# Performance work log

Measured on AMD Instinct MI355X. Metric: run time of the kernel, lower is better.

Reference implementation:

```python
import jax, jax.numpy as jnp
import numpy as np

B, T, E, H, M2 = 8, 2048, 256, 2, 134
HD = E // H


def setup_inputs() -> dict:
    key = jax.random.key(0)
    ks = jax.random.split(key, 10)
    s = 0.02
    return {
        "X": jax.random.normal(ks[0], (B, T, E), dtype=jnp.float32),
        "Y": jax.random.uniform(ks[1], (B, M2), dtype=jnp.float32),
        "wpe": s * jax.random.normal(ks[2], (T, E), dtype=jnp.float32),
        "ln1_g": jnp.ones((E,), jnp.float32), "ln1_b": jnp.zeros((E,), jnp.float32),
        "attn_w": s * jax.random.normal(ks[3], (3 * E, E), dtype=jnp.float32),
        "attn_b": jnp.zeros((3 * E,), jnp.float32),
        "attnproj_w": s * jax.random.normal(ks[4], (E, E), dtype=jnp.float32),
        "attnproj_b": jnp.zeros((E,), jnp.float32),
        "ln2_g": jnp.ones((E,), jnp.float32), "ln2_b": jnp.zeros((E,), jnp.float32),
        "fc_w": s * jax.random.normal(ks[5], (2 * E, E), dtype=jnp.float32),
        "fc_b": jnp.zeros((2 * E,), jnp.float32),
        "mlpproj_w": s * jax.random.normal(ks[6], (E, 2 * E), dtype=jnp.float32),
        "mlpproj_b": jnp.zeros((E,), jnp.float32),
        "lnf_g": jnp.ones((E,), jnp.float32), "lnf_b": jnp.zeros((E,), jnp.float32),
        "head_w": s * jax.random.normal(ks[7], (M2, E), dtype=jnp.float32),
        "head_b": jnp.zeros((M2,), jnp.float32),
    }


def _ln(x, g, b, eps=1e-5):
    mu = x.mean(-1, keepdims=True)
    var = ((x - mu) ** 2).mean(-1, keepdims=True)
    return (x - mu) * jax.lax.rsqrt(var + eps) * g + b


def reference(X, Y, wpe, ln1_g, ln1_b, attn_w, attn_b, attnproj_w, attnproj_b,
              ln2_g, ln2_b, fc_w, fc_b, mlpproj_w, mlpproj_b, lnf_g, lnf_b,
              head_w, head_b):
    # positional ids = arange(T) -> wpe itself; cls ids = [0]*T/2 + [1]*T/2
    cls_ids = np.concatenate([np.zeros(T // 2, np.int32), np.ones(T // 2, np.int32)])
    x = X + wpe + wpe[cls_ids]                      # [B,T,E] (dropout = identity, eval)

    # single Block (n_layer=1), preceded by ReLU as in cross_mod loop
    x = jax.nn.relu(x)
    h = _ln(x, ln1_g, ln1_b)
    qkv = h @ attn_w.T + attn_b                     # [B,T,3E]
    q, k, v = jnp.split(qkv, 3, axis=-1)
    q, k, v = jax.nn.relu(q), jax.nn.relu(k), jax.nn.relu(v)
    split_heads = lambda t: t.reshape(B, T, H, HD).transpose(0, 2, 1, 3)
    q, k, v = split_heads(q), split_heads(k), split_heads(v)
    att = jnp.einsum('bhqd,bhkd->bhqk', q, k) * (1.0 / np.sqrt(HD))
    tril = jnp.tril(jnp.ones((T, T), dtype=bool))
    # masked_fill(-inf) then ReLU  ==  zero outside causal mask, ReLU inside
    att = jnp.where(tril, jax.nn.relu(att), 0.0)    # [B,H,T,T]
    y = jnp.einsum('bhqk,bhkd->bhqd', att, v)
    y = y.transpose(0, 2, 1, 3).reshape(B, T, E)
    x = x + (y @ attnproj_w.T + attnproj_b)

    h = _ln(x, ln2_g, ln2_b)
    x = x + (jax.nn.relu(h @ fc_w.T + fc_b) @ mlpproj_w.T + mlpproj_b)

    x = jax.nn.relu(x)
    x = _ln(x, lnf_g, lnf_b)
    x = jax.nn.relu(x)
    emb = x.mean(axis=1)                            # [B,E]
    logits = jax.nn.relu(emb @ head_w.T + head_b)   # [B,M2]

    loss1 = jnp.sqrt(jnp.mean((logits - Y) ** 2))
    e1, e2 = emb[:, : E // 2], emb[:, E // 2:]
    loss3 = jnp.sqrt(jnp.mean((e1 - e2) ** 2))
    loss = 50.0 * loss1 + loss3
    return (e1, e2, loss, loss1, loss3, logits)
```

## Files before the change

### kernel.cpp

```cpp
#include <hip/hip_runtime.h>
#include <hip/hip_bf16.h>

#define Bc 8
#define Tc 2048
#define Ec 256
#define Hc 2
#define HDc 128
#define Mrows (Bc*Tc)
#define M2c 134

using bfx8  = __attribute__((ext_vector_type(8))) __bf16;
using f32x4 = __attribute__((ext_vector_type(4))) float;

__device__ __forceinline__ void gll16(const __bf16* g, __bf16* lds) {
    __builtin_amdgcn_global_load_lds(
        (const __attribute__((address_space(1))) unsigned int*)g,
        (__attribute__((address_space(3))) unsigned int*)lds, 16, 0, 0);
}

__global__ __launch_bounds__(256) void prep_k(const float* attn_w, const float* apw,
                                              const float* fcw, const float* mpw,
                                              __bf16* wb, float* embsum) {
    int i = blockIdx.x * 256 + threadIdx.x;
    if (i < 2048) embsum[i] = 0.f;
    if (i < 196608)       wb[i] = (__bf16)attn_w[i];
    else if (i < 262144)  wb[i] = (__bf16)apw[i - 196608];
    else if (i < 393216)  wb[i] = (__bf16)fcw[i - 262144];
    else if (i < 524288)  wb[i] = (__bf16)mpw[i - 393216];
}

__global__ __launch_bounds__(256) void embed_ln_k(const float* X, const float* wpe,
                                                  const float* g, const float* bb,
                                                  __bf16* xres, __bf16* hb) {
    int m = blockIdx.x;
    int t = m & (Tc - 1);
    int e = threadIdx.x;
    float v = X[(size_t)m * Ec + e] + wpe[(size_t)t * Ec + e] + wpe[(size_t)(t >= 1024) * Ec + e];
    v = fmaxf(v, 0.f);
    xres[(size_t)m * Ec + e] = (__bf16)v;
    float s1 = v, s2 = v * v;
    #pragma unroll
    for (int o = 32; o; o >>= 1) { s1 += __shfl_xor(s1, o, 64); s2 += __shfl_xor(s2, o, 64); }
    __shared__ float a1[4], a2[4];
    int w = threadIdx.x >> 6;
    if ((threadIdx.x & 63) == 0) { a1[w] = s1; a2[w] = s2; }
    __syncthreads();
    float m1 = (a1[0] + a1[1] + a1[2] + a1[3]) * (1.f / 256.f);
    float m2 = (a2[0] + a2[1] + a2[2] + a2[3]) * (1.f / 256.f);
    float r = rsqrtf(m2 - m1 * m1 + 1e-5f);
    hb[(size_t)m * Ec + e] = (__bf16)((v - m1) * r * g[e] + bb[e]);
}

template <int EPI>
__global__ __launch_bounds__(256) void gemm_bt(const __bf16* __restrict__ A,
                                               const __bf16* __restrict__ Bw,
                                               const float* __restrict__ bias,
                                               int N, int K,
                                               __bf16* __restrict__ outb,
                                               __bf16* __restrict__ Qb,
                                               __bf16* __restrict__ Kb,
                                               __bf16* __restrict__ Vb) {
    __shared__ __bf16 As[128 * 64];
    __shared__ __bf16 Bs[128 * 64];
    const int tid = threadIdx.x, w = tid >> 6, l = tid & 63;
    const int m0 = blockIdx.y * 128, n0 = blockIdx.x * 128;
    const int wr = w >> 1, wc = w & 1;
    const int quad = l >> 4, col15 = l & 15;

    f32x4 acc[4][4];
    f32x4 zz = {0.f, 0.f, 0.f, 0.f};
    #pragma unroll
    for (int i = 0; i < 4; i++)
        #pragma unroll
        for (int j = 0; j < 4; j++) acc[i][j] = zz;

    const int lrow = l >> 3;
    const int pbs  = l & 7;

    for (int kb = 0; kb < K; kb += 64) {
        #pragma unroll
        for (int it = 0; it < 4; it++) {
            int chunk = w * 4 + it;
            int row = chunk * 8 + lrow;
            int lb = pbs ^ (row & 7);
            gll16(A  + (size_t)(m0 + row) * K + kb + lb * 8, As + chunk * 512);
            gll16(Bw + (size_t)(n0 + row) * K + kb + lb * 8, Bs + chunk * 512);
        }
        __syncthreads();
        #pragma unroll
        for (int ks = 0; ks < 2; ks++) {
            bfx8 af[4], bfr[4];
            #pragma unroll
            for (int rt = 0; rt < 4; rt++) {
                int row = wr * 64 + rt * 16 + col15;
                int pb = (ks * 4 + quad) ^ (row & 7);
                af[rt] = *(const bfx8*)(As + row * 64 + pb * 8);
            }
            #pragma unroll
            for (int ct = 0; ct < 4; ct++) {
                int row = wc * 64 + ct * 16 + col15;
                int pb = (ks * 4 + quad) ^ (row & 7);
                bfr[ct] = *(const bfx8*)(Bs + row * 64 + pb * 8);
            }
            #pragma unroll
            for (int rt = 0; rt < 4; rt++)
                #pragma unroll
                for (int ct = 0; ct < 4; ct++)
                    acc[rt][ct] = __builtin_amdgcn_mfma_f32_16x16x32_bf16(af[rt], bfr[ct], acc[rt][ct], 0, 0, 0);
        }
        __syncthreads();
    }

    #pragma unroll
    for (int rt = 0; rt < 4; rt++)
        #pragma unroll
        for (int ct = 0; ct < 4; ct++) {
            int mgb = m0 + wr * 64 + rt * 16 + quad * 4;
            int ng  = n0 + wc * 64 + ct * 16 + col15;
            float bsv = bias[ng];
            #pragma unroll
            for (int r = 0; r < 4; r++) {
                float val = acc[rt][ct][r] + bsv;
                int mg = mgb + r;
                if constexpr (EPI == 0) {
                    val = fmaxf(val, 0.f);
                    int sel = ng >> 8;
                    int hh = (ng >> 7) & 1;
                    int d = ng & 127;
                    int bb = mg >> 11, tt = mg & (Tc - 1);
                    size_t idx = ((size_t)((bb * 2 + hh) * Tc + tt)) * HDc + d;
                    __bf16 bv = (__bf16)val;
                    if (sel == 0) Qb[idx] = bv;
                    else if (sel == 1) Kb[idx] = bv;
                    else Vb[idx] = bv;
                } else {
                    outb[(size_t)mg * 512 + ng] = (__bf16)fmaxf(val, 0.f);
                }
            }
        }
}

__global__ __launch_bounds__(256) void transpose_v(const unsigned short* Vb, unsigned short* Vt) {
    __shared__ unsigned short tile[64][66];
    int kt = blockIdx.x, dt = blockIdx.y, bh = blockIdx.z;
    int tid = threadIdx.x;
    int k0 = kt * 64, d0 = dt * 64;
    int rr = tid >> 4, cc = (tid & 15) * 4;
    #pragma unroll
    for (int p = 0; p < 4; p++) {
        int k = p * 16 + rr;
        const unsigned short* src = Vb + ((size_t)(bh * Tc + k0 + k)) * HDc + d0 + cc;
        ushort4 vv = *(const ushort4*)src;
        tile[k][cc] = vv.x; tile[k][cc + 1] = vv.y; tile[k][cc + 2] = vv.z; tile[k][cc + 3] = vv.w;
    }
    __syncthreads();
    #pragma unroll
    for (int p = 0; p < 4; p++) {
        int d = p * 16 + rr;
        unsigned short* dst = Vt + ((size_t)(bh * HDc + d0 + d)) * Tc + k0 + cc;
        ushort4 ov;
        ov.x = tile[cc][d]; ov.y = tile[cc + 1][d]; ov.z = tile[cc + 2][d]; ov.w = tile[cc + 3][d];
        *(ushort4*)dst = ov;
    }
}

__global__ __launch_bounds__(256, 4) void attn6_k(const __bf16* __restrict__ Qb,
                                                  const __bf16* __restrict__ Kb,
                                                  const __bf16* __restrict__ Vt,
                                                  __bf16* __restrict__ Y1,
                                                  __bf16* __restrict__ Y2,
                                                  __bf16* __restrict__ Y3,
                                                  __bf16* __restrict__ Y4) {
    __shared__ __bf16 Ks[64 * 128];
    __shared__ __bf16 Vs[128 * 64];
    __shared__ __bf16 Ss[64 * 64];
    int bid = blockIdx.x;
    int lane8 = bid & 7;
    int s = bid >> 3;
    int bh = ((s & 1) << 3) | lane8;
    int f = s >> 1;
    int qt, ch;
    if (f < 8)       { qt = f;                    ch = 0; }
    else if (f < 24) { qt = 8 + ((f - 8) >> 1);   ch = (f - 8) & 1; }
    else if (f < 48) { int r = f - 24; int d3 = r / 3; qt = 16 + d3; ch = r - 3 * d3; }
    else             { int r = f - 48; qt = 24 + (r >> 2); ch = r & 3; }
    int Q0 = qt * 64;
    int kts = ch * 8;
    int kte = min(kts + 8, qt + 1);

    int tid = threadIdx.x, w = tid >> 6, l = tid & 63;
    int quad = l >> 4, col15 = l & 15;
    const int lrowK = l >> 4, pbsK = l & 15;
    const int lrowV = l >> 3, pbsV = l & 7;

    #pragma unroll
    for (int it = 0; it < 4; it++) {
        int chunk = w * 4 + it;
        int row = chunk * 4 + lrowK;
        int lb = pbsK ^ (row & 7);
        gll16(Qb + ((size_t)(bh * Tc + Q0 + row)) * HDc + lb * 8, Ks + chunk * 512);
    }
    __syncthreads();
    bfx8 qf[4];
    #pragma unroll
    for (int ks = 0; ks < 4; ks++) {
        int row = w * 16 + col15;
        int pb = (ks * 4 + quad) ^ (row & 7);
        qf[ks] = *(const bfx8*)(Ks + row * 128 + pb * 8);
    }

    f32x4 zz = {0.f, 0.f, 0.f, 0.f};
    f32x4 yacc[8];
    #pragma unroll
    for (int i = 0; i < 8; i++) yacc[i] = zz;

    for (int kt = kts; kt < kte; kt++) {
        __syncthreads();
        #pragma unroll
        for (int it = 0; it < 4; it++) {
            int chunk = w * 4 + it;
            int rowK = chunk * 4 + lrowK;
            int lbK = pbsK ^ (rowK & 7);
            gll16(Kb + ((size_t)(bh * Tc + kt * 64 + rowK)) * HDc + lbK * 8, Ks + chunk * 512);
            int rowV = chunk * 8 + lrowV;
            int lbV = pbsV ^ (rowV & 7);
            gll16(Vt + ((size_t)(bh * HDc + rowV)) * Tc + kt * 64 + lbV * 8, Vs + chunk * 512);
        }
        __syncthreads();

        f32x4 sacc[4];
        #pragma unroll
        for (int i = 0; i < 4; i++) sacc[i] = zz;
        #pragma unroll
        for (int ks = 0; ks < 4; ks++) {
            #pragma unroll
            for (int ct = 0; ct < 4; ct++) {
                int row = ct * 16 + col15;
                int pb = (ks * 4 + quad) ^ (row & 7);
                bfx8 kf = *(const bfx8*)(Ks + row * 128 + pb * 8);
                sacc[ct] = __builtin_amdgcn_mfma_f32_16x16x32_bf16(qf[ks], kf, sacc[ct], 0, 0, 0);
            }
        }

        #pragma unroll
        for (int ct = 0; ct < 4; ct++) {
            int kl = ct * 16 + col15;
            int kg = kt * 64 + kl;
            int blk = kl >> 3, off = kl & 7;
            #pragma unroll
            for (int r = 0; r < 4; r++) {
                int qlw = w * 16 + quad * 4 + r;
                float val = (kg <= Q0 + qlw) ? fmaxf(sacc[ct][r], 0.f) : 0.f;
                int pb = blk ^ (qlw & 7);
                Ss[qlw * 64 + pb * 8 + off] = (__bf16)val;
            }
        }

        #pragma unroll
        for (int ks = 0; ks < 2; ks++) {
            int rowS = w * 16 + col15;
            int pbS = (ks * 4 + quad) ^ (rowS & 7);
            bfx8 sf = *(const bfx8*)(Ss + rowS * 64 + pbS * 8);
            #pragma unroll
            for (int dt = 0; dt < 8; dt++) {
                int row = dt * 16 + col15;
                int pb = (ks * 4 + quad) ^ (row & 7);
                bfx8 vf = *(const bfx8*)(Vs + row * 64 + pb * 8);
                yacc[dt] = __builtin_amdgcn_mfma_f32_16x16x32_bf16(sf, vf, yacc[dt], 0, 0, 0);
            }
        }
    }

    __bf16* Yp = (ch == 0) ? Y1 : (ch == 1) ? Y2 : (ch == 2) ? Y3 : Y4;
    int b = bh >> 1, h = bh & 1;
    const float sc = 0.08838834764831845f;
    #pragma unroll
    for (int dt = 0; dt < 8; dt++) {
        int d = dt * 16 + col15;
        #pragma unroll
        for (int r = 0; r < 4; r++) {
            int q = Q0 + w * 16 + quad * 4 + r;
            Yp[((size_t)(b * Tc + q)) * Ec + h * HDc + d] = (__bf16)(yacc[dt][r] * sc);
        }
    }
}

template <int MODE>
__global__ __launch_bounds__(256) void gemm_ln(const __bf16* __restrict__ A,
                                               const __bf16* __restrict__ A2,
                                               const __bf16* __restrict__ A3,
                                               const __bf16* __restrict__ A4,
                                               const __bf16* __restrict__ W,
                                               const float* __restrict__ bias, int K,
                                               const __bf16* __restrict__ resid,
                                               const float* __restrict__ g,
                                               const float* __restrict__ bb,
                                               __bf16* __restrict__ out1,
                                               __bf16* __restrict__ out2,
                                               float* __restrict__ embsum) {
    __shared__ __bf16 As[64 * 64];
    __shared__ __bf16 Bs[256 * 64];
    __shared__ float cs[256];
    const int tid = threadIdx.x, w = tid >> 6, l = tid & 63;
    const int m0 = blockIdx.x * 64;
    const int quad = l >> 4, col15 = l & 15;
    const int lrow = l >> 3, pbs = l & 7;

    f32x4 acc[16];
    f32x4 zz = {0.f, 0.f, 0.f, 0.f};
    #pragma unroll
    for (int i = 0; i < 16; i++) acc[i] = zz;
    if (MODE == 1) { cs[tid] = 0.f; }

    int nsum = 1;
    if (MODE == 0) nsum = (((m0 & (Tc - 1)) >> 6) + 8) >> 3;
    const __bf16* Ys[4] = {A, A2, A3, A4};

    for (int kb = 0; kb < K; kb += 64) {
        if (MODE == 0) {
            bfx8 av[2];
            int rows[2], blks[2];
            #pragma unroll
            for (int it = 0; it < 2; it++) {
                int idx = it * 256 + tid;
                int row = idx >> 3, blk = idx & 7;
                rows[it] = row; blks[it] = blk;
                size_t off = (size_t)(m0 + row) * K + kb + blk * 8;
                bfx8 a1 = *(const bfx8*)(A + off);
                float tmp[8];
                #pragma unroll
                for (int jj = 0; jj < 8; jj++) tmp[jj] = (float)a1[jj];
                for (int j = 1; j < nsum; j++) {
                    bfx8 aj = *(const bfx8*)(Ys[j] + off);
                    #pragma unroll
                    for (int jj = 0; jj < 8; jj++) tmp[jj] += (float)aj[jj];
                }
                #pragma unroll
                for (int jj = 0; jj < 8; jj++) a1[jj] = (__bf16)tmp[jj];
                av[it] = a1;
            }
            __syncthreads();
            #pragma unroll
            for (int it = 0; it < 2; it++) {
                int row = rows[it];
                int pb = blks[it] ^ (row & 7);
                *(bfx8*)(As + row * 64 + pb * 8) = av[it];
            }
        } else {
            __syncthreads();
            #pragma unroll
            for (int it = 0; it < 2; it++) {
                int chunk = w * 2 + it;
                int row = chunk * 8 + lrow;
                int lb = pbs ^ (row & 7);
                gll16(A + (size_t)(m0 + row) * K + kb + lb * 8, As + chunk * 512);
            }
        }
        #pragma unroll
        for (int it = 0; it < 8; it++) {
            int chunk = w * 8 + it;
            int row = chunk * 8 + lrow;
            int lb = pbs ^ (row & 7);
            gll16(W + (size_t)row * K + kb + lb * 8, Bs + chunk * 512);
        }
        __syncthreads();
        #pragma unroll
        for (int ks = 0; ks < 2; ks++) {
            int arow = w * 16 + col15;
            int apb = (ks * 4 + quad) ^ (arow & 7);
            bfx8 af = *(const bfx8*)(As + arow * 64 + apb * 8);
            #pragma unroll
            for (int ct = 0; ct < 16; ct++) {
                int brow = ct * 16 + col15;
                int bpb = (ks * 4 + quad) ^ (brow & 7);
                bfx8 bf = *(const bfx8*)(Bs + brow * 64 + bpb * 8);
                acc[ct] = __builtin_amdgcn_mfma_f32_16x16x32_bf16(af, bf, acc[ct], 0, 0, 0);
            }
        }
    }
    __syncthreads();

    float xv[16][4];
    #pragma unroll
    for (int ct = 0; ct < 16; ct++) {
        int ng = ct * 16 + col15;
        float bsv = bias[ng];
        #pragma unroll
        for (int r = 0; r < 4; r++) {
            int mg = m0 + w * 16 + quad * 4 + r;
            float v = acc[ct][r] + bsv + (float)resid[(size_t)mg * 256 + ng];
            if (MODE == 1) v = fmaxf(v, 0.f);
            xv[ct][r] = v;
        }
    }
    if (MODE == 0) {
        #pragma unroll
        for (int ct = 0; ct < 16; ct++) {
            int ng = ct * 16 + col15;
            #pragma unroll
            for (int r = 0; r < 4; r++) {
                int mg = m0 + w * 16 + quad * 4 + r;
                out1[(size_t)mg * 256 + ng] = (__bf16)xv[ct][r];
            }
        }
    }
    float s1[4], s2[4];
    #pragma unroll
    for (int r = 0; r < 4; r++) {
        float a = 0.f, b2 = 0.f;
        #pragma unroll
        for (int ct = 0; ct < 16; ct++) { a += xv[ct][r]; b2 += xv[ct][r] * xv[ct][r]; }
        #pragma unroll
        for (int o = 1; o < 16; o <<= 1) { a += __shfl_xor(a, o, 64); b2 += __shfl_xor(b2, o, 64); }
        s1[r] = a; s2[r] = b2;
    }
    float colsum[16];
    #pragma unroll
    for (int ct = 0; ct < 16; ct++) colsum[ct] = 0.f;
    #pragma unroll
    for (int r = 0; r < 4; r++) {
        float mu = s1[r] * (1.f / 256.f);
        float var = s2[r] * (1.f / 256.f) - mu * mu;
        float rs = rsqrtf(var + 1e-5f);
        #pragma unroll
        for (int ct = 0; ct < 16; ct++) {
            int ng = ct * 16 + col15;
            float h = (xv[ct][r] - mu) * rs * g[ng] + bb[ng];
            if (MODE == 1) {
                colsum[ct] += fmaxf(h, 0.f);
            } else {
                int mg = m0 + w * 16 + quad * 4 + r;
                out2[(size_t)mg * 256 + ng] = (__bf16)h;
            }
        }
    }
    if (MODE == 1) {
        #pragma unroll
        for (int ct = 0; ct < 16; ct++) {
            colsum[ct] += __shfl_xor(colsum[ct], 16, 64);
            colsum[ct] += __shfl_xor(colsum[ct], 32, 64);
        }
        if (quad == 0) {
            #pragma unroll
            for (int ct = 0; ct < 16; ct++)
                atomicAdd(&cs[ct * 16 + col15], colsum[ct]);
        }
        __syncthreads();
        atomicAdd(&embsum[(m0 >> 11) * 256 + tid], cs[tid]);
    }
}

__global__ __launch_bounds__(256) void final_k(const float* embsum, const float* Yt,
                                               const float* head_w, const float* head_b,
                                               float* out) {
    __shared__ float semb[2048];
    __shared__ float slog[1072];
    int tid = threadIdx.x;
    for (int i = tid; i < 2048; i += 256) semb[i] = embsum[i] * (1.f / 2048.f);
    __syncthreads();
    float part1 = 0.f;
    for (int idx = tid; idx < 1072; idx += 256) {
        int b = idx / M2c, n = idx - b * M2c;
        float acc = head_b[n];
        const float* wn = head_w + (size_t)n * Ec;
        const float* e = semb + b * Ec;
        #pragma unroll 8
        for (int k = 0; k < Ec; k++) acc += e[k] * wn[k];
        acc = fmaxf(acc, 0.f);
        slog[idx] = acc;
        float d = acc - Yt[idx];
        part1 += d * d;
    }
    float part3 = 0.f;
    for (int idx = tid; idx < 1024; idx += 256) {
        int b = idx >> 7, i = idx & 127;
        float d = semb[b * Ec + i] - semb[b * Ec + 128 + i];
        part3 += d * d;
    }
    #pragma unroll
    for (int o = 32; o; o >>= 1) { part1 += __shfl_xor(part1, o, 64); part3 += __shfl_xor(part3, o, 64); }
    __shared__ float r1[4], r3[4];
    int w = tid >> 6;
    if ((tid & 63) == 0) { r1[w] = part1; r3[w] = part3; }
    __syncthreads();
    float l1 = sqrtf((r1[0] + r1[1] + r1[2] + r1[3]) / 1072.f);
    float l3 = sqrtf((r3[0] + r3[1] + r3[2] + r3[3]) / 1024.f);
    for (int idx = tid; idx < 1024; idx += 256) {
        int b = idx >> 7, i = idx & 127;
        out[idx]        = semb[b * Ec + i];
        out[1024 + idx] = semb[b * Ec + 128 + i];
    }
    if (tid == 0) {
        out[2048] = 50.f * l1 + l3;
        out[2049] = l1;
        out[2050] = l3;
    }
    for (int idx = tid; idx < 1072; idx += 256) out[2051 + idx] = slog[idx];
}

extern "C" void kernel_launch(void* const* d_in, const int* in_sizes, int n_in,
                              void* d_out, int out_size, void* d_ws, size_t ws_size,
                              hipStream_t stream) {
    const float* X        = (const float*)d_in[0];
    const float* Yt       = (const float*)d_in[1];
    const float* wpe      = (const float*)d_in[2];
    const float* ln1_g    = (const float*)d_in[3];
    const float* ln1_b    = (const float*)d_in[4];
    const float* attn_w   = (const float*)d_in[5];
    const float* attn_b   = (const float*)d_in[6];
    const float* apw      = (const float*)d_in[7];
    const float* apb      = (const float*)d_in[8];
    const float* ln2_g    = (const float*)d_in[9];
    const float* ln2_b    = (const float*)d_in[10];
    const float* fcw      = (const float*)d_in[11];
    const float* fcb      = (const float*)d_in[12];
    const float* mpw      = (const float*)d_in[13];
    const float* mpb      = (const float*)d_in[14];
    const float* lnf_g    = (const float*)d_in[15];
    const float* lnf_b    = (const float*)d_in[16];
    const float* head_w   = (const float*)d_in[17];
    const float* head_b   = (const float*)d_in[18];

    char* ws = (char*)d_ws;
    const size_t MB = 1048576;
    __bf16* xres   = (__bf16*)(ws + 0 * MB);
    __bf16* hb     = (__bf16*)(ws + 8 * MB);
    __bf16* Qb     = (__bf16*)(ws + 16 * MB);
    __bf16* Kb     = (__bf16*)(ws + 24 * MB);
    __bf16* Vb     = (__bf16*)(ws + 32 * MB);
    __bf16* Vt     = (__bf16*)(ws + 40 * MB);
    __bf16* Y1     = (__bf16*)(ws + 48 * MB);
    __bf16* Y2     = (__bf16*)(ws + 56 * MB);
    __bf16* fcout  = (__bf16*)(ws + 64 * MB);
    __bf16* wb     = (__bf16*)(ws + 80 * MB);
    float*  embsum = (float*)(ws + 81 * MB);

    __bf16* x2   = Qb;
    __bf16* h2   = Kb;
    __bf16* Y3   = hb;
    __bf16* Y4   = Vb;

    __bf16* wqkv = wb;
    __bf16* wap  = wb + 196608;
    __bf16* wfc  = wb + 262144;
    __bf16* wmp  = wb + 393216;

    prep_k<<<2048, 256, 0, stream>>>(attn_w, apw, fcw, mpw, wb, embsum);
    embed_ln_k<<<Mrows, 256, 0, stream>>>(X, wpe, ln1_g, ln1_b, xres, hb);
    gemm_bt<0><<<dim3(6, 128), 256, 0, stream>>>(hb, wqkv, attn_b, 768, 256,
                                                 nullptr, Qb, Kb, Vb);
    transpose_v<<<dim3(32, 2, 16), 256, 0, stream>>>((const unsigned short*)Vb, (unsigned short*)Vt);
    attn6_k<<<1280, 256, 0, stream>>>(Qb, Kb, Vt, Y1, Y2, Y3, Y4);
    gemm_ln<0><<<256, 256, 0, stream>>>(Y1, Y2, Y3, Y4, wap, apb, 256, xres, ln2_g, ln2_b,
                                        x2, h2, nullptr);
    gemm_bt<2><<<dim3(4, 128), 256, 0, stream>>>(h2, wfc, fcb, 512, 256,
                                                 fcout, nullptr, nullptr, nullptr);
    gemm_ln<1><<<256, 256, 0, stream>>>(fcout, nullptr, nullptr, nullptr, wmp, mpb, 512,
                                        x2, lnf_g, lnf_b, nullptr, nullptr, embsum);
    final_k<<<1, 256, 0, stream>>>(embsum, Yt, head_w, head_b, (float*)d_out);
}
```

Baseline: 256.6 us.

## Fuse attention-proj, LN2, MLP and final LN into one kernel; merge prep into embed

Replaces the three post-attention kernels (proj+LN2, fc GEMM, mlp-proj+LNf) with one kernel per 64-row tile. The LN2 output and the fc activations stay in LDS instead of going through global memory. The weight-conversion prep kernel is folded into the embedding/LN kernel to drop one launch. This removes intermediate HBM traffic and launches, but uses only 256 blocks at one block per CU with large LDS (~120KB), and each block re-streams all MLP weights through LDS.

```diff
diff --git a/kernel.cpp b/kernel.cpp
--- a/kernel.cpp
+++ b/kernel.cpp
@@ -18,23 +18,23 @@
         (__attribute__((address_space(3))) unsigned int*)lds, 16, 0, 0);
 }
 
-__global__ __launch_bounds__(256) void prep_k(const float* attn_w, const float* apw,
-                                              const float* fcw, const float* mpw,
-                                              __bf16* wb, float* embsum) {
-    int i = blockIdx.x * 256 + threadIdx.x;
-    if (i < 2048) embsum[i] = 0.f;
-    if (i < 196608)       wb[i] = (__bf16)attn_w[i];
-    else if (i < 262144)  wb[i] = (__bf16)apw[i - 196608];
-    else if (i < 393216)  wb[i] = (__bf16)fcw[i - 262144];
-    else if (i < 524288)  wb[i] = (__bf16)mpw[i - 393216];
-}
-
-__global__ __launch_bounds__(256) void embed_ln_k(const float* X, const float* wpe,
-                                                  const float* g, const float* bb,
-                                                  __bf16* xres, __bf16* hb) {
+__global__ __launch_bounds__(256) void embed_prep_k(const float* X, const float* wpe,
+                                                    const float* g, const float* bb,
+                                                    const float* attn_w, const float* apw,
+                                                    const float* fcw, const float* mpw,
+                                                    __bf16* wb, float* embsum,
+                                                    __bf16* xres, __bf16* hb) {
     int m = blockIdx.x;
+    int e = threadIdx.x;
+    if (m < 2048) {
+        int i = m * 256 + e;
+        if (i < 196608)       wb[i] = (__bf16)attn_w[i];
+        else if (i < 262144)  wb[i] = (__bf16)apw[i - 196608];
+        else if (i < 393216)  wb[i] = (__bf16)fcw[i - 262144];
+        else                  wb[i] = (__bf16)mpw[i - 393216];
+        if (m < 8) embsum[m * 256 + e] = 0.f;
+    }
     int t = m & (Tc - 1);
-    int e = threadIdx.x;
     float v = X[(size_t)m * Ec + e] + wpe[(size_t)t * Ec + e] + wpe[(size_t)(t >= 1024) * Ec + e];
     v = fmaxf(v, 0.f);
     xres[(size_t)m * Ec + e] = (__bf16)v;
@@ -51,15 +51,13 @@
     hb[(size_t)m * Ec + e] = (__bf16)((v - m1) * r * g[e] + bb[e]);
 }
 
-template <int EPI>
-__global__ __launch_bounds__(256) void gemm_bt(const __bf16* __restrict__ A,
-                                               const __bf16* __restrict__ Bw,
-                                               const float* __restrict__ bias,
-                                               int N, int K,
-                                               __bf16* __restrict__ outb,
-                                               __bf16* __restrict__ Qb,
-                                               __bf16* __restrict__ Kb,
-                                               __bf16* __restrict__ Vb) {
+__global__ __launch_bounds__(256) void gemm_qkv(const __bf16* __restrict__ A,
+                                                const __bf16* __restrict__ Bw,
+                                                const float* __restrict__ bias,
+                                                __bf16* __restrict__ Qb,
+                                                __bf16* __restrict__ Kb,
+                                                __bf16* __restrict__ Vb) {
+    const int K = 256;
     __shared__ __bf16 As[128 * 64];
     __shared__ __bf16 Bs[128 * 64];
     const int tid = threadIdx.x, w = tid >> 6, l = tid & 63;
@@ -120,22 +118,17 @@
             float bsv = bias[ng];
             #pragma unroll
             for (int r = 0; r < 4; r++) {
-                float val = acc[rt][ct][r] + bsv;
+                float val = fmaxf(acc[rt][ct][r] + bsv, 0.f);
                 int mg = mgb + r;
-                if constexpr (EPI == 0) {
-                    val = fmaxf(val, 0.f);
-                    int sel = ng >> 8;
-                    int hh = (ng >> 7) & 1;
-                    int d = ng & 127;
-                    int bb = mg >> 11, tt = mg & (Tc - 1);
-                    size_t idx = ((size_t)((bb * 2 + hh) * Tc + tt)) * HDc + d;
-                    __bf16 bv = (__bf16)val;
-                    if (sel == 0) Qb[idx] = bv;
-                    else if (sel == 1) Kb[idx] = bv;
-                    else Vb[idx] = bv;
-                } else {
-                    outb[(size_t)mg * 512 + ng] = (__bf16)fmaxf(val, 0.f);
-                }
+                int sel = ng >> 8;
+                int hh = (ng >> 7) & 1;
+                int d = ng & 127;
+                int bb = mg >> 11, tt = mg & (Tc - 1);
+                size_t idx = ((size_t)((bb * 2 + hh) * Tc + tt)) * HDc + d;
+                __bf16 bv = (__bf16)val;
+                if (sel == 0) Qb[idx] = bv;
+                else if (sel == 1) Kb[idx] = bv;
+                else Vb[idx] = bv;
             }
         }
 }
@@ -285,90 +278,82 @@
     }
 }
 
-template <int MODE>
-__global__ __launch_bounds__(256) void gemm_ln(const __bf16* __restrict__ A,
-                                               const __bf16* __restrict__ A2,
-                                               const __bf16* __restrict__ A3,
-                                               const __bf16* __restrict__ A4,
-                                               const __bf16* __restrict__ W,
-                                               const float* __restrict__ bias, int K,
-                                               const __bf16* __restrict__ resid,
-                                               const float* __restrict__ g,
-                                               const float* __restrict__ bb,
-                                               __bf16* __restrict__ out1,
-                                               __bf16* __restrict__ out2,
-                                               float* __restrict__ embsum) {
-    __shared__ __bf16 As[64 * 64];
+__global__ __launch_bounds__(256, 1) void mega_k(const __bf16* __restrict__ Y1,
+                                                 const __bf16* __restrict__ Y2,
+                                                 const __bf16* __restrict__ Y3,
+                                                 const __bf16* __restrict__ Y4,
+                                                 const __bf16* __restrict__ wap,
+                                                 const float* __restrict__ apb,
+                                                 const __bf16* __restrict__ xres,
+                                                 const float* __restrict__ ln2_g,
+                                                 const float* __restrict__ ln2_b,
+                                                 const __bf16* __restrict__ wfc,
+                                                 const float* __restrict__ fcb,
+                                                 const __bf16* __restrict__ wmp,
+                                                 const float* __restrict__ mpb,
+                                                 const float* __restrict__ lnf_g,
+                                                 const float* __restrict__ lnf_b,
+                                                 float* __restrict__ embsum) {
+    __shared__ __bf16 h2s[4 * 4096];
+    __shared__ __bf16 fc64[8 * 4096];
     __shared__ __bf16 Bs[256 * 64];
     __shared__ float cs[256];
     const int tid = threadIdx.x, w = tid >> 6, l = tid & 63;
     const int m0 = blockIdx.x * 64;
     const int quad = l >> 4, col15 = l & 15;
     const int lrow = l >> 3, pbs = l & 7;
+    f32x4 zz = {0.f, 0.f, 0.f, 0.f};
+    cs[tid] = 0.f;
+
+    int nsum = (((m0 & (Tc - 1)) >> 6) + 8) >> 3;
+    const __bf16* Ys[4] = {Y1, Y2, Y3, Y4};
+    __bf16* As = fc64;
 
     f32x4 acc[16];
-    f32x4 zz = {0.f, 0.f, 0.f, 0.f};
     #pragma unroll
     for (int i = 0; i < 16; i++) acc[i] = zz;
-    if (MODE == 1) { cs[tid] = 0.f; }
-
-    int nsum = 1;
-    if (MODE == 0) nsum = (((m0 & (Tc - 1)) >> 6) + 8) >> 3;
-    const __bf16* Ys[4] = {A, A2, A3, A4};
-
-    for (int kb = 0; kb < K; kb += 64) {
-        if (MODE == 0) {
-            bfx8 av[2];
-            int rows[2], blks[2];
-            #pragma unroll
-            for (int it = 0; it < 2; it++) {
-                int idx = it * 256 + tid;
-                int row = idx >> 3, blk = idx & 7;
-                rows[it] = row; blks[it] = blk;
-                size_t off = (size_t)(m0 + row) * K + kb + blk * 8;
-                bfx8 a1 = *(const bfx8*)(A + off);
-                float tmp[8];
+
+    for (int kb = 0; kb < 256; kb += 64) {
+        bfx8 av[2]; int rows[2], blks[2];
+        #pragma unroll
+        for (int it = 0; it < 2; it++) {
+            int idx = it * 256 + tid;
+            int row = idx >> 3, blk = idx & 7;
+            rows[it] = row; blks[it] = blk;
+            size_t off = (size_t)(m0 + row) * 256 + kb + blk * 8;
+            bfx8 a1 = *(const bfx8*)(Y1 + off);
+            float tmp[8];
+            #pragma unroll
+            for (int jj = 0; jj < 8; jj++) tmp[jj] = (float)a1[jj];
+            for (int j = 1; j < nsum; j++) {
+                bfx8 aj = *(const bfx8*)(Ys[j] + off);
                 #pragma unroll
-                for (int jj = 0; jj < 8; jj++) tmp[jj] = (float)a1[jj];
-                for (int j = 1; j < nsum; j++) {
-                    bfx8 aj = *(const bfx8*)(Ys[j] + off);
-                    #pragma unroll
-                    for (int jj = 0; jj < 8; jj++) tmp[jj] += (float)aj[jj];
-                }
-                #pragma unroll
-                for (int jj = 0; jj < 8; jj++) a1[jj] = (__bf16)tmp[jj];
-                av[it] = a1;
-            }
-            __syncthreads();
-            #pragma unroll
-            for (int it = 0; it < 2; it++) {
-                int row = rows[it];
-                int pb = blks[it] ^ (row & 7);
-                *(bfx8*)(As + row * 64 + pb * 8) = av[it];
-            }
-        } else {
-            __syncthreads();
-            #pragma unroll
-            for (int it = 0; it < 2; it++) {
-                int chunk = w * 2 + it;
-                int row = chunk * 8 + lrow;
-                int lb = pbs ^ (row & 7);
-                gll16(A + (size_t)(m0 + row) * K + kb + lb * 8, As + chunk * 512);
-            }
+                for (int jj = 0; jj < 8; jj++) tmp[jj] += (float)aj[jj];
+            }
+            #pragma unroll
+            for (int jj = 0; jj < 8; jj++) a1[jj] = (__bf16)tmp[jj];
+            av[it] = a1;
+        }
+        __syncthreads();
+        #pragma unroll
+        for (int it = 0; it < 2; it++) {
+            int row = rows[it];
+            int pb = blks[it] ^ (row & 7);
+            *(bfx8*)(As + row * 64 + pb * 8) = av[it];
         }
         #pragma unroll
         for (int it = 0; it < 8; it++) {
             int chunk = w * 8 + it;
             int row = chunk * 8 + lrow;
             int lb = pbs ^ (row & 7);
-            gll16(W + (size_t)row * K + kb + lb * 8, Bs + chunk * 512);
+            gll16(wap + (size_t)row * 256 + kb + lb * 8, Bs + chunk * 512);
         }
         __syncthreads();
         #pragma unroll
         for (int ks = 0; ks < 2; ks++) {
             int arow = w * 16 + col15;
-            int apb = (ks * 4 + quad) ^ (arow & 7);
-            bfx8 af = *(const bfx8*)(As + arow * 64 + apb * 8);
+            int apbk = (ks * 4 + quad) ^ (arow & 7);
+            bfx8 af = *(const bfx8*)(As + arow * 64 + apbk * 8);
             #pragma unroll
             for (int ct = 0; ct < 16; ct++) {
                 int brow = ct * 16 + col15;
@@ -378,31 +363,123 @@
             }
         }
     }
-    __syncthreads();
 
     float xv[16][4];
     #pragma unroll
     for (int ct = 0; ct < 16; ct++) {
         int ng = ct * 16 + col15;
-        float bsv = bias[ng];
+        float bsv = apb[ng];
         #pragma unroll
         for (int r = 0; r < 4; r++) {
             int mg = m0 + w * 16 + quad * 4 + r;
-            float v = acc[ct][r] + bsv + (float)resid[(size_t)mg * 256 + ng];
-            if (MODE == 1) v = fmaxf(v, 0.f);
-            xv[ct][r] = v;
-        }
-    }
-    if (MODE == 0) {
+            xv[ct][r] = acc[ct][r] + bsv + (float)xres[(size_t)mg * 256 + ng];
+        }
+    }
+    {
+        float s1[4], s2[4];
+        #pragma unroll
+        for (int r = 0; r < 4; r++) {
+            float a = 0.f, b2 = 0.f;
+            #pragma unroll
+            for (int ct = 0; ct < 16; ct++) { a += xv[ct][r]; b2 += xv[ct][r] * xv[ct][r]; }
+            #pragma unroll
+            for (int o = 1; o < 16; o <<= 1) { a += __shfl_xor(a, o, 64); b2 += __shfl_xor(b2, o, 64); }
+            s1[r] = a; s2[r] = b2;
+        }
+        #pragma unroll
+        for (int r = 0; r < 4; r++) {
+            float mu = s1[r] * (1.f / 256.f);
+            float var = s2[r] * (1.f / 256.f) - mu * mu;
+            float rs = rsqrtf(var + 1e-5f);
+            int row = w * 16 + quad * 4 + r;
+            #pragma unroll
+            for (int ct = 0; ct < 16; ct++) {
+                int ng = ct * 16 + col15;
+                float h = (xv[ct][r] - mu) * rs * ln2_g[ng] + ln2_b[ng];
+                int panel = ng >> 6, c = ng & 63;
+                h2s[panel * 4096 + row * 64 + ((c >> 3) ^ (row & 7)) * 8 + (c & 7)] = (__bf16)h;
+            }
+        }
+    }
+
+    for (int half = 0; half < 2; half++) {
+        f32x4 acc2[16];
+        #pragma unroll
+        for (int i = 0; i < 16; i++) acc2[i] = zz;
+        for (int kb = 0; kb < 256; kb += 64) {
+            __syncthreads();
+            #pragma unroll
+            for (int it = 0; it < 8; it++) {
+                int chunk = w * 8 + it;
+                int row = chunk * 8 + lrow;
+                int lb = pbs ^ (row & 7);
+                gll16(wfc + (size_t)(half * 256 + row) * 256 + kb + lb * 8, Bs + chunk * 512);
+            }
+            __syncthreads();
+            int panel = kb >> 6;
+            #pragma unroll
+            for (int ks = 0; ks < 2; ks++) {
+                int arow = w * 16 + col15;
+                int apbk = (ks * 4 + quad) ^ (arow & 7);
+                bfx8 af = *(const bfx8*)(h2s + panel * 4096 + arow * 64 + apbk * 8);
+                #pragma unroll
+                for (int ct = 0; ct < 16; ct++) {
+                    int brow = ct * 16 + col15;
+                    int bpb = (ks * 4 + quad) ^ (brow & 7);
+                    bfx8 bf = *(const bfx8*)(Bs + brow * 64 + bpb * 8);
+                    acc2[ct] = __builtin_amdgcn_mfma_f32_16x16x32_bf16(af, bf, acc2[ct], 0, 0, 0);
+                }
+            }
+        }
         #pragma unroll
         for (int ct = 0; ct < 16; ct++) {
-            int ng = ct * 16 + col15;
+            int col = half * 256 + ct * 16 + col15;
+            float bsv = fcb[col];
+            int panel = col >> 6, c = col & 63;
             #pragma unroll
             for (int r = 0; r < 4; r++) {
-                int mg = m0 + w * 16 + quad * 4 + r;
-                out1[(size_t)mg * 256 + ng] = (__bf16)xv[ct][r];
-            }
-        }
+                int row = w * 16 + quad * 4 + r;
+                float val = fmaxf(acc2[ct][r] + bsv, 0.f);
+                fc64[panel * 4096 + row * 64 + ((c >> 3) ^ (row & 7)) * 8 + (c & 7)] = (__bf16)val;
+            }
+        }
+    }
+
+    #pragma unroll
+    for (int i = 0; i < 16; i++) acc[i] = zz;
+    for (int kb = 0; kb < 512; kb += 64) {
+        __syncthreads();
+        #pragma unroll
+        for (int it = 0; it < 8; it++) {
+            int chunk = w * 8 + it;
+            int row = chunk * 8 + lrow;
+            int lb = pbs ^ (row & 7);
+            gll16(wmp + (size_t)row * 512 + kb + lb * 8, Bs + chunk * 512);
+        }
+        __syncthreads();
+        int panel = kb >> 6;
+        #pragma unroll
+        for (int ks = 0; ks < 2; ks++) {
+            int arow = w * 16 + col15;
+            int apbk = (ks * 4 + quad) ^ (arow & 7);
+            bfx8 af = *(const bfx8*)(fc64 + panel * 4096 + arow * 64 + apbk * 8);
+            #pragma unroll
+            for (int ct = 0; ct < 16; ct++) {
+                int brow = ct * 16 + col15;
+                int bpb = (ks * 4 + quad) ^ (brow & 7);
+                bfx8 bf = *(const bfx8*)(Bs + brow * 64 + bpb * 8);
+                acc[ct] = __builtin_amdgcn_mfma_f32_16x16x32_bf16(af, bf, acc[ct], 0, 0, 0);
+            }
+        }
+    }
+
+    #pragma unroll
+    for (int ct = 0; ct < 16; ct++) {
+        int ng = ct * 16 + col15;
+        float bsv = mpb[ng];
+        #pragma unroll
+        for (int r = 0; r < 4; r++)
+            xv[ct][r] = fmaxf(acc[ct][r] + bsv + xv[ct][r], 0.f);
     }
     float s1[4], s2[4];
     #pragma unroll
@@ -425,29 +502,22 @@
         #pragma unroll
         for (int ct = 0; ct < 16; ct++) {
             int ng = ct * 16 + col15;
-            float h = (xv[ct][r] - mu) * rs * g[ng] + bb[ng];
-            if (MODE == 1) {
-                colsum[ct] += fmaxf(h, 0.f);
-            } else {
-                int mg = m0 + w * 16 + quad * 4 + r;
-                out2[(size_t)mg * 256 + ng] = (__bf16)h;
-            }
-        }
-    }
-    if (MODE == 1) {
-        #pragma unroll
-        for (int ct = 0; ct < 16; ct++) {
-            colsum[ct] += __shfl_xor(colsum[ct], 16, 64);
-            colsum[ct] += __shfl_xor(colsum[ct], 32, 64);
-        }
-        if (quad == 0) {
-            #pragma unroll
-            for (int ct = 0; ct < 16; ct++)
-                atomicAdd(&cs[ct * 16 + col15], colsum[ct]);
-        }
-        __syncthreads();
-        atomicAdd(&embsum[(m0 >> 11) * 256 + tid], cs[tid]);
-    }
+            float h = (xv[ct][r] - mu) * rs * lnf_g[ng] + lnf_b[ng];
+            colsum[ct] += fmaxf(h, 0.f);
+        }
+    }
+    #pragma unroll
+    for (int ct = 0; ct < 16; ct++) {
+        colsum[ct] += __shfl_xor(colsum[ct], 16, 64);
+        colsum[ct] += __shfl_xor(colsum[ct], 32, 64);
+    }
+    if (quad == 0) {
+        #pragma unroll
+        for (int ct = 0; ct < 16; ct++)
+            atomicAdd(&cs[ct * 16 + col15], colsum[ct]);
+    }
+    __syncthreads();
+    atomicAdd(&embsum[(m0 >> 11) * 256 + tid], cs[tid]);
 }
 
 __global__ __launch_bounds__(256) void final_k(const float* embsum, const float* Yt,
@@ -531,31 +601,23 @@
     __bf16* Vt     = (__bf16*)(ws + 40 * MB);
     __bf16* Y1     = (__bf16*)(ws + 48 * MB);
     __bf16* Y2     = (__bf16*)(ws + 56 * MB);
-    __bf16* fcout  = (__bf16*)(ws + 64 * MB);
-    __bf16* wb     = (__bf16*)(ws + 80 * MB);
-    float*  embsum = (float*)(ws + 81 * MB);
-
-    __bf16* x2   = Qb;
-    __bf16* h2   = Kb;
-    __bf16* Y3   = hb;
-    __bf16* Y4   = Vb;
+    __bf16* wb     = (__bf16*)(ws + 64 * MB);
+    float*  embsum = (float*)(ws + 65 * MB);
+
+    __bf16* Y3 = hb;
+    __bf16* Y4 = Vb;
 
     __bf16* wqkv = wb;
     __bf16* wap  = wb + 196608;
     __bf16* wfc  = wb + 262144;
     __bf16* wmp  = wb + 393216;
 
-    prep_k<<<2048, 256, 0, stream>>>(attn_w, apw, fcw, mpw, wb, embsum);
-    embed_ln_k<<<Mrows, 256, 0, stream>>>(X, wpe, ln1_g, ln1_b, xres, hb);
-    gemm_bt<0><<<dim3(6, 128), 256, 0, stream>>>(hb, wqkv, attn_b, 768, 256,
-                                                 nullptr, Qb, Kb, Vb);
+    embed_prep_k<<<Mrows, 256, 0, stream>>>(X, wpe, ln1_g, ln1_b,
+                                            attn_w, apw, fcw, mpw, wb, embsum, xres, hb);
+    gemm_qkv<<<dim3(6, 128), 256, 0, stream>>>(hb, wqkv, attn_b, Qb, Kb, Vb);
     transpose_v<<<dim3(32, 2, 16), 256, 0, stream>>>((const unsigned short*)Vb, (unsigned short*)Vt);
     attn6_k<<<1280, 256, 0, stream>>>(Qb, Kb, Vt, Y1, Y2, Y3, Y4);
-    gemm_ln<0><<<256, 256, 0, stream>>>(Y1, Y2, Y3, Y4, wap, apb, 256, xres, ln2_g, ln2_b,
-                                        x2, h2, nullptr);
-    gemm_bt<2><<<dim3(4, 128), 256, 0, stream>>>(h2, wfc, fcb, 512, 256,
-                                                 fcout, nullptr, nullptr, nullptr);
-    gemm_ln<1><<<256, 256, 0, stream>>>(fcout, nullptr, nullptr, nullptr, wmp, mpb, 512,
-                                        x2, lnf_g, lnf_b, nullptr, nullptr, embsum);
+    mega_k<<<256, 256, 0, stream>>>(Y1, Y2, Y3, Y4, wap, apb, xres, ln2_g, ln2_b,
+                                    wfc, fcb, wmp, mpb, lnf_g, lnf_b, embsum);
     final_k<<<1, 256, 0, stream>>>(embsum, Yt, head_w, head_b, (float*)d_out);
 }
```

Measured after the change: 250.4 us. -2.4%, faster.
